# Kernel tuning notes

Hardware: AMD Instinct MI355X
Metric: run time of the kernel (lower is better)

The kernel has to match this reference:

```python
import jax, jax.numpy as jnp
import numpy as np

NUM_ENTS = 20000
NUM_RELS = 500
DIM = 256
BATCH = 32
GAMMA = 12.0
EPSILON = 2.0
EMB_RANGE = (GAMMA + EPSILON) / DIM  # embedding_range
PI = 3.1415926235897933


def setup_inputs() -> dict:
    key = jax.random.key(0)
    k1, k2, k3, k4 = jax.random.split(key, 4)
    # xavier_normal for 2-D params: std = sqrt(2/(fan_in+fan_out))
    std_e = float(np.sqrt(2.0 / (NUM_ENTS + 2 * DIM)))
    std_r = float(np.sqrt(2.0 / (NUM_RELS + 3 * DIM)))
    emb_e = jax.random.normal(k1, (NUM_ENTS, 2 * DIM), dtype=jnp.float32) * std_e
    emb_rel = jax.random.normal(k2, (NUM_RELS, 3 * DIM), dtype=jnp.float32) * std_r
    e1 = jax.random.randint(k3, (BATCH,), 0, NUM_ENTS, dtype=jnp.int32)
    rel = jax.random.randint(k4, (BATCH,), 0, NUM_RELS, dtype=jnp.int32)
    e2_multi = jax.random.uniform(jax.random.fold_in(key, 7), (BATCH, NUM_ENTS), dtype=jnp.float32)
    phase_weight = jnp.full((1, 1), 0.5 * EMB_RANGE, dtype=jnp.float32)
    modulus_weight = jnp.full((1, 1), 1.0, dtype=jnp.float32)
    return {
        "g": 0,
        "e1": e1,
        "rel": rel,
        "e2_multi": e2_multi,
        "emb_e": emb_e,
        "emb_rel": emb_rel,
        "phase_weight": phase_weight,
        "modulus_weight": modulus_weight,
    }


def reference(g, e1, rel, e2_multi, emb_e, emb_rel, phase_weight, modulus_weight):
    head = emb_e[e1]            # (B, 2D)
    r = emb_rel[rel]            # (B, 3D)
    tail = emb_e                # (N, 2D)

    phase_head, mod_head = jnp.split(head, 2, axis=-1)            # (B, D) each
    phase_rel, mod_rel, bias_rel = jnp.split(r, 3, axis=-1)       # (B, D) each
    phase_tail, mod_tail = jnp.split(tail, 2, axis=-1)            # (N, D) each

    scale = EMB_RANGE / PI
    phase_head = phase_head / scale
    phase_rel = phase_rel / scale
    phase_tail = phase_tail / scale

    # (B, N, D) broadcast
    phase_score = (phase_head + phase_rel)[:, None, :] - phase_tail[None, :, :]

    mod_rel = jnp.abs(mod_rel)
    bias_rel = jnp.minimum(bias_rel, 1.0)
    bias_rel = jnp.where(bias_rel < -mod_rel, -mod_rel, bias_rel)

    r_score = (mod_head * (mod_rel + bias_rel))[:, None, :] \
        - mod_tail[None, :, :] * (1.0 - bias_rel)[:, None, :]      # (B, N, D)

    phase_term = jnp.sum(jnp.abs(jnp.sin(phase_score / 2.0)), axis=-1) * phase_weight  # (B, N)
    r_term = jnp.linalg.norm(r_score, axis=-1) * modulus_weight                          # (B, N)

    return jax.nn.sigmoid(GAMMA - (phase_term + r_term))
```

## Files before the change

### kernel.cpp

```cpp
#include <hip/hip_runtime.h>
#include <math.h>


#define D_   256
#define N_   20000
#define NT   16
#define NBLK (N_ / NT)

#define K2S 4.571428571428571f

#define WS_A1 0
#define WS_A2 16384
#define WS_SC 32768
#define WS_S0 65536

typedef short short8 __attribute__((ext_vector_type(8)));
typedef float f32x4  __attribute__((ext_vector_type(4)));
typedef _Float16 half2_t __attribute__((ext_vector_type(2)));

union PKH { unsigned u; half2_t h; };

__device__ __forceinline__ float sinrev_(float x) { return __builtin_amdgcn_sinf(x); }
__device__ __forceinline__ float cosrev_(float x) { return __builtin_amdgcn_cosf(x); }

__device__ __forceinline__ unsigned short bf16r(float x) {
    union { float f; unsigned u; } v; v.f = x;
    return (unsigned short)((v.u + 0x7FFFu + ((v.u >> 16) & 1u)) >> 16);
}

__device__ __forceinline__ short8 pack8(float4 a, float4 b, bool sq) {
    float v[8] = {a.x, a.y, a.z, a.w, b.x, b.y, b.z, b.w};
    short8 r;
#pragma unroll
    for (int i = 0; i < 8; ++i) { float x = sq ? v[i] * v[i] : v[i]; r[i] = (short)bf16r(x); }
    return r;
}

__global__ __launch_bounds__(256)
void hake_prep(const int* __restrict__ e1, const int* __restrict__ rel,
               const float* __restrict__ emb_e, const float* __restrict__ emb_rel,
               char* __restrict__ ws)
{
    __shared__ float sp[4];
    const int b = blockIdx.x, d = threadIdx.x;
    const int he = e1[b], hr = rel[b];
    const float ph = emb_e[(size_t)he * 512 + d];
    const float mh = emb_e[(size_t)he * 512 + 256 + d];
    const float pr = emb_rel[(size_t)hr * 768 + d];
    const float mr = emb_rel[(size_t)hr * 768 + 256 + d];
    const float bi = emb_rel[(size_t)hr * 768 + 512 + d];

    const float a = (ph + pr) * K2S;
    PKH x;
    x.h.x = (_Float16)(-cosrev_(a));
    x.h.y = (_Float16)(sinrev_(a));
    ((unsigned*)(ws + WS_SC))[b * 256 + d] = x.u;

    const float mra = fabsf(mr);
    float bic = fminf(bi, 1.0f);
    bic = (bic < -mra) ? -mra : bic;
    const float cc  = 1.0f - bic;
    const float mhp = mh * (mra + bic);
    ((short*)(ws + WS_A1))[b * 256 + d] = (short)bf16r(cc * cc);
    ((short*)(ws + WS_A2))[b * 256 + d] = (short)bf16r(-2.0f * mhp * cc);

    float s0 = mhp * mhp;
#pragma unroll
    for (int o = 1; o < 64; o <<= 1) s0 += __shfl_xor(s0, o, 64);
    if ((threadIdx.x & 63) == 0) sp[threadIdx.x >> 6] = s0;
    __syncthreads();
    if (threadIdx.x == 0)
        ((float*)(ws + WS_S0))[b] = sp[0] + sp[1] + sp[2] + sp[3];
}

__global__ __launch_bounds__(512, 8)
void hake_main(const float* __restrict__ emb_e,
               const char* __restrict__ ws,
               const float* __restrict__ pw_p, const float* __restrict__ mw_p,
               float* __restrict__ out)
{
    __shared__ unsigned Pb[NT * 256];
    __shared__ float U[4352];

    const int t   = threadIdx.x;
    const int l   = t & 63;
    const int w   = t >> 6;
    const int b   = t & 31;
    const int g   = t >> 5;
    const int dlo = g * 16;
    const int fr  = l & 15;
    const int hi  = l >> 4;
    const int n0  = blockIdx.x * NT;

    const short*    A1w = (const short*)(ws + WS_A1);
    const short*    A2w = (const short*)(ws + WS_A2);
    const unsigned* SCw = (const unsigned*)(ws + WS_SC);
    const float*    S0w = (const float*)(ws + WS_S0);

    const int term  = w >> 2;
    const int dbase = (w & 3) * 64;
    const float* mtp = emb_e + (size_t)(n0 + fr) * (2 * D_) + D_;
    float4 bva0 = *(const float4*)(mtp + dbase + hi * 8);
    float4 bvb0 = *(const float4*)(mtp + dbase + hi * 8 + 4);
    float4 bva1 = *(const float4*)(mtp + dbase + 32 + hi * 8);
    float4 bvb1 = *(const float4*)(mtp + dbase + 32 + hi * 8 + 4);

    const float* prow0 = emb_e + (size_t)(n0 + w * 2) * (2 * D_);
    const float* prow1 = emb_e + (size_t)(n0 + w * 2 + 1) * (2 * D_);
    float2 lp00 = *(const float2*)(prow0 + 2 * l);
    float2 lp01 = *(const float2*)(prow0 + 128 + 2 * l);
    float2 lp10 = *(const float2*)(prow1 + 2 * l);
    float2 lp11 = *(const float2*)(prow1 + 128 + 2 * l);

    const short* At = term ? A2w : A1w;
    short8 a00 = *(const short8*)(At + fr * 256 + dbase + hi * 8);
    short8 a01 = *(const short8*)(At + fr * 256 + dbase + 32 + hi * 8);
    short8 a10 = *(const short8*)(At + (16 + fr) * 256 + dbase + hi * 8);
    short8 a11 = *(const short8*)(At + (16 + fr) * 256 + dbase + 32 + hi * 8);

    {
        PKH w0, w1;
        float v0, v1;
        v0 = lp00.x * K2S; v1 = lp00.y * K2S;
        w0.h.x = (_Float16)sinrev_(v0); w0.h.y = (_Float16)cosrev_(v0);
        w1.h.x = (_Float16)sinrev_(v1); w1.h.y = (_Float16)cosrev_(v1);
        *(uint2*)(&Pb[(w * 2) * 256 + 2 * l]) = make_uint2(w0.u, w1.u);
        v0 = lp01.x * K2S; v1 = lp01.y * K2S;
        w0.h.x = (_Float16)sinrev_(v0); w0.h.y = (_Float16)cosrev_(v0);
        w1.h.x = (_Float16)sinrev_(v1); w1.h.y = (_Float16)cosrev_(v1);
        *(uint2*)(&Pb[(w * 2) * 256 + 128 + 2 * l]) = make_uint2(w0.u, w1.u);
        v0 = lp10.x * K2S; v1 = lp10.y * K2S;
        w0.h.x = (_Float16)sinrev_(v0); w0.h.y = (_Float16)cosrev_(v0);
        w1.h.x = (_Float16)sinrev_(v1); w1.h.y = (_Float16)cosrev_(v1);
        *(uint2*)(&Pb[(w * 2 + 1) * 256 + 2 * l]) = make_uint2(w0.u, w1.u);
        v0 = lp11.x * K2S; v1 = lp11.y * K2S;
        w0.h.x = (_Float16)sinrev_(v0); w0.h.y = (_Float16)cosrev_(v0);
        w1.h.x = (_Float16)sinrev_(v1); w1.h.y = (_Float16)cosrev_(v1);
        *(uint2*)(&Pb[(w * 2 + 1) * 256 + 128 + 2 * l]) = make_uint2(w0.u, w1.u);
    }

    {
        short8 bf0 = pack8(bva0, bvb0, term == 0);
        short8 bf1 = pack8(bva1, bvb1, term == 0);
        f32x4 acc0 = {0.f, 0.f, 0.f, 0.f};
        f32x4 acc1 = {0.f, 0.f, 0.f, 0.f};
        acc0 = __builtin_amdgcn_mfma_f32_16x16x32_bf16(a00, bf0, acc0, 0, 0, 0);
        acc0 = __builtin_amdgcn_mfma_f32_16x16x32_bf16(a01, bf1, acc0, 0, 0, 0);
        acc1 = __builtin_amdgcn_mfma_f32_16x16x32_bf16(a10, bf0, acc1, 0, 0, 0);
        acc1 = __builtin_amdgcn_mfma_f32_16x16x32_bf16(a11, bf1, acc1, 0, 0, 0);
#pragma unroll
        for (int r = 0; r < 4; ++r) {
            U[(w * 32 + hi * 4 + r) * 17 + fr]      = acc0[r];
            U[(w * 32 + 16 + hi * 4 + r) * 17 + fr] = acc1[r];
        }
    }
    __syncthreads();

    const int fn = t >> 5, fb = t & 31;
    float rr = 0.0f;
#pragma unroll
    for (int ww = 0; ww < 8; ++ww) rr += U[(ww * 32 + fb) * 17 + fn];

    half2_t Xr[16];
    {
        uint4 s0 = *(const uint4*)(SCw + b * 256 + dlo);
        uint4 s1 = *(const uint4*)(SCw + b * 256 + dlo + 4);
        uint4 s2 = *(const uint4*)(SCw + b * 256 + dlo + 8);
        uint4 s3 = *(const uint4*)(SCw + b * 256 + dlo + 12);
        Xr[0]  = __builtin_bit_cast(half2_t, s0.x);
        Xr[1]  = __builtin_bit_cast(half2_t, s0.y);
        Xr[2]  = __builtin_bit_cast(half2_t, s0.z);
        Xr[3]  = __builtin_bit_cast(half2_t, s0.w);
        Xr[4]  = __builtin_bit_cast(half2_t, s1.x);
        Xr[5]  = __builtin_bit_cast(half2_t, s1.y);
        Xr[6]  = __builtin_bit_cast(half2_t, s1.z);
        Xr[7]  = __builtin_bit_cast(half2_t, s1.w);
        Xr[8]  = __builtin_bit_cast(half2_t, s2.x);
        Xr[9]  = __builtin_bit_cast(half2_t, s2.y);
        Xr[10] = __builtin_bit_cast(half2_t, s2.z);
        Xr[11] = __builtin_bit_cast(half2_t, s2.w);
        Xr[12] = __builtin_bit_cast(half2_t, s3.x);
        Xr[13] = __builtin_bit_cast(half2_t, s3.y);
        Xr[14] = __builtin_bit_cast(half2_t, s3.z);
        Xr[15] = __builtin_bit_cast(half2_t, s3.w);
    }

    float sph[NT];
#pragma unroll
    for (int j = 0; j < NT; ++j) sph[j] = 0.0f;

#pragma unroll
    for (int q = 0; q < 4; ++q) {
        const half2_t x0 = Xr[q * 4 + 0];
        const half2_t x1 = Xr[q * 4 + 1];
        const half2_t x2 = Xr[q * 4 + 2];
        const half2_t x3 = Xr[q * 4 + 3];
#pragma unroll
        for (int j = 0; j < NT; ++j) {
            uint4 tv = *(const uint4*)(&Pb[j * 256 + dlo + q * 4]);
            sph[j] += fabsf(__builtin_amdgcn_fdot2(x0, __builtin_bit_cast(half2_t, tv.x), 0.0f, false));
            sph[j] += fabsf(__builtin_amdgcn_fdot2(x1, __builtin_bit_cast(half2_t, tv.y), 0.0f, false));
            sph[j] += fabsf(__builtin_amdgcn_fdot2(x2, __builtin_bit_cast(half2_t, tv.z), 0.0f, false));
            sph[j] += fabsf(__builtin_amdgcn_fdot2(x3, __builtin_bit_cast(half2_t, tv.w), 0.0f, false));
        }
    }

#pragma unroll
    for (int j = 0; j < NT; ++j) sph[j] += __shfl_xor(sph[j], 32, 64);
    __syncthreads();
    if (l < 32) {
#pragma unroll
        for (int j = 0; j < NT; ++j) U[(w * 16 + j) * 32 + l] = sph[j];
    }
    __syncthreads();

    {
        float pa = 0.0f;
#pragma unroll
        for (int ww = 0; ww < 8; ++ww) pa += U[(ww * 16 + fn) * 32 + fb];
        float rfull = fmaxf(rr + S0w[fb], 0.0f);
        float z = fmaf(pa, pw_p[0], sqrtf(rfull) * mw_p[0]) - 12.0f;
        out[(size_t)fb * N_ + (n0 + fn)] = 1.0f / (1.0f + __expf(z));
    }
}

extern "C" void kernel_launch(void* const* d_in, const int* in_sizes, int n_in,
                              void* d_out, int out_size, void* d_ws, size_t ws_size,
                              hipStream_t stream)
{
    const int*   e1      = (const int*)d_in[1];
    const int*   rel     = (const int*)d_in[2];
    const float* emb_e   = (const float*)d_in[4];
    const float* emb_rel = (const float*)d_in[5];
    const float* pw      = (const float*)d_in[6];
    const float* mw      = (const float*)d_in[7];
    float* out = (float*)d_out;

    hipLaunchKernelGGL(hake_prep, dim3(32), dim3(256), 0, stream,
                       e1, rel, emb_e, emb_rel, (char*)d_ws);
    hipLaunchKernelGGL(hake_main, dim3(NBLK), dim3(512), 0, stream,
                       emb_e, (const char*)d_ws, pw, mw, out);
}
```

Baseline: 35.40 us.

## Move modulus MFMA GEMM into a separate kernel and transpose the phase workspace

The modulus term (bf16 MFMA over the tail modulus against A1/A2) moves out of hake_main into a new hake_rgemm kernel. That kernel does the full K=256 reduction per 16-row wave, adds S0, and writes a 32xN result matrix to workspace; hake_main then just prefetches one value per thread. The per-batch phase vectors are stored transposed so each thread loads its Xr registers with coalesced scalar loads. The aim is a lighter main kernel with fewer shared-memory reductions and one fewer barrier, paid for with an extra launch and a roughly 2.5 MB global write and read round trip. The phase reduction now uses float4 stores to a stride-17 shared array, which may be misaligned.

```diff
diff --git a/kernel.cpp b/kernel.cpp
--- a/kernel.cpp
+++ b/kernel.cpp
@@ -11,8 +11,9 @@
 
 #define WS_A1 0
 #define WS_A2 16384
-#define WS_SC 32768
+#define WS_XT 32768
 #define WS_S0 65536
+#define WS_R  65792
 
 typedef short short8 __attribute__((ext_vector_type(8)));
 typedef float f32x4  __attribute__((ext_vector_type(4)));
@@ -54,7 +55,7 @@
     PKH x;
     x.h.x = (_Float16)(-cosrev_(a));
     x.h.y = (_Float16)(sinrev_(a));
-    ((unsigned*)(ws + WS_SC))[b * 256 + d] = x.u;
+    ((unsigned*)(ws + WS_XT))[d * 32 + b] = x.u;
 
     const float mra = fabsf(mr);
     float bic = fminf(bi, 1.0f);
@@ -73,6 +74,50 @@
         ((float*)(ws + WS_S0))[b] = sp[0] + sp[1] + sp[2] + sp[3];
 }
 
+__global__ __launch_bounds__(256)
+void hake_rgemm(const float* __restrict__ emb_e, char* __restrict__ ws)
+{
+    const int t = threadIdx.x;
+    const int w = t >> 6, l = t & 63;
+    const int n0 = blockIdx.x * 64 + w * 16;
+    if (n0 >= N_) return;
+
+    const short* A1w = (const short*)(ws + WS_A1);
+    const short* A2w = (const short*)(ws + WS_A2);
+    const float* S0w = (const float*)(ws + WS_S0);
+    float*       Rw  = (float*)(ws + WS_R);
+
+    const int fr   = l & 15;
+    const int koff = (l >> 4) * 8;
+    const float* mtp = emb_e + (size_t)(n0 + fr) * (2 * D_) + D_;
+
+    f32x4 acc0 = {0.f, 0.f, 0.f, 0.f};
+    f32x4 acc1 = {0.f, 0.f, 0.f, 0.f};
+#pragma unroll
+    for (int ch = 0; ch < 8; ++ch) {
+        const int d = ch * 32 + koff;
+        float4 va = *(const float4*)(mtp + d);
+        float4 vb = *(const float4*)(mtp + d + 4);
+        short8 b2f = pack8(va, vb, false);
+        short8 b1f = pack8(va, vb, true);
+        short8 a1_0 = *(const short8*)(A1w + fr * 256 + d);
+        short8 a2_0 = *(const short8*)(A2w + fr * 256 + d);
+        short8 a1_1 = *(const short8*)(A1w + (16 + fr) * 256 + d);
+        short8 a2_1 = *(const short8*)(A2w + (16 + fr) * 256 + d);
+        acc0 = __builtin_amdgcn_mfma_f32_16x16x32_bf16(a1_0, b1f, acc0, 0, 0, 0);
+        acc0 = __builtin_amdgcn_mfma_f32_16x16x32_bf16(a2_0, b2f, acc0, 0, 0, 0);
+        acc1 = __builtin_amdgcn_mfma_f32_16x16x32_bf16(a1_1, b1f, acc1, 0, 0, 0);
+        acc1 = __builtin_amdgcn_mfma_f32_16x16x32_bf16(a2_1, b2f, acc1, 0, 0, 0);
+    }
+
+#pragma unroll
+    for (int r = 0; r < 4; ++r) {
+        const int row = (l >> 4) * 4 + r;
+        Rw[(size_t)row * N_ + n0 + fr]        = acc0[r] + S0w[row];
+        Rw[(size_t)(16 + row) * N_ + n0 + fr] = acc1[r] + S0w[16 + row];
+    }
+}
+
 __global__ __launch_bounds__(512, 8)
 void hake_main(const float* __restrict__ emb_e,
                const char* __restrict__ ws,
@@ -80,7 +125,7 @@
                float* __restrict__ out)
 {
     __shared__ unsigned Pb[NT * 256];
-    __shared__ float U[4352];
+    __shared__ float redf[8 * 32 * 17];
 
     const int t   = threadIdx.x;
     const int l   = t & 63;
@@ -88,22 +133,14 @@
     const int b   = t & 31;
     const int g   = t >> 5;
     const int dlo = g * 16;
-    const int fr  = l & 15;
-    const int hi  = l >> 4;
     const int n0  = blockIdx.x * NT;
 
-    const short*    A1w = (const short*)(ws + WS_A1);
-    const short*    A2w = (const short*)(ws + WS_A2);
-    const unsigned* SCw = (const unsigned*)(ws + WS_SC);
-    const float*    S0w = (const float*)(ws + WS_S0);
-
-    const int term  = w >> 2;
-    const int dbase = (w & 3) * 64;
-    const float* mtp = emb_e + (size_t)(n0 + fr) * (2 * D_) + D_;
-    float4 bva0 = *(const float4*)(mtp + dbase + hi * 8);
-    float4 bvb0 = *(const float4*)(mtp + dbase + hi * 8 + 4);
-    float4 bva1 = *(const float4*)(mtp + dbase + 32 + hi * 8);
-    float4 bvb1 = *(const float4*)(mtp + dbase + 32 + hi * 8 + 4);
+    const unsigned* XTw = (const unsigned*)(ws + WS_XT);
+    const float*    Rw  = (const float*)(ws + WS_R);
+
+    const int fn = t & 15, fb = t >> 4;
+
+    float rprefetch = Rw[(size_t)fb * N_ + n0 + fn];
 
     const float* prow0 = emb_e + (size_t)(n0 + w * 2) * (2 * D_);
     const float* prow1 = emb_e + (size_t)(n0 + w * 2 + 1) * (2 * D_);
@@ -112,11 +149,10 @@
     float2 lp10 = *(const float2*)(prow1 + 2 * l);
     float2 lp11 = *(const float2*)(prow1 + 128 + 2 * l);
 
-    const short* At = term ? A2w : A1w;
-    short8 a00 = *(const short8*)(At + fr * 256 + dbase + hi * 8);
-    short8 a01 = *(const short8*)(At + fr * 256 + dbase + 32 + hi * 8);
-    short8 a10 = *(const short8*)(At + (16 + fr) * 256 + dbase + hi * 8);
-    short8 a11 = *(const short8*)(At + (16 + fr) * 256 + dbase + 32 + hi * 8);
+    half2_t Xr[16];
+#pragma unroll
+    for (int i = 0; i < 16; ++i)
+        Xr[i] = __builtin_bit_cast(half2_t, XTw[(dlo + i) * 32 + b]);
 
     {
         PKH w0, w1;
@@ -138,52 +174,7 @@
         w1.h.x = (_Float16)sinrev_(v1); w1.h.y = (_Float16)cosrev_(v1);
         *(uint2*)(&Pb[(w * 2 + 1) * 256 + 128 + 2 * l]) = make_uint2(w0.u, w1.u);
     }
-
-    {
-        short8 bf0 = pack8(bva0, bvb0, term == 0);
-        short8 bf1 = pack8(bva1, bvb1, term == 0);
-        f32x4 acc0 = {0.f, 0.f, 0.f, 0.f};
-        f32x4 acc1 = {0.f, 0.f, 0.f, 0.f};
-        acc0 = __builtin_amdgcn_mfma_f32_16x16x32_bf16(a00, bf0, acc0, 0, 0, 0);
-        acc0 = __builtin_amdgcn_mfma_f32_16x16x32_bf16(a01, bf1, acc0, 0, 0, 0);
-        acc1 = __builtin_amdgcn_mfma_f32_16x16x32_bf16(a10, bf0, acc1, 0, 0, 0);
-        acc1 = __builtin_amdgcn_mfma_f32_16x16x32_bf16(a11, bf1, acc1, 0, 0, 0);
-#pragma unroll
-        for (int r = 0; r < 4; ++r) {
-            U[(w * 32 + hi * 4 + r) * 17 + fr]      = acc0[r];
-            U[(w * 32 + 16 + hi * 4 + r) * 17 + fr] = acc1[r];
-        }
-    }
     __syncthreads();
-
-    const int fn = t >> 5, fb = t & 31;
-    float rr = 0.0f;
-#pragma unroll
-    for (int ww = 0; ww < 8; ++ww) rr += U[(ww * 32 + fb) * 17 + fn];
-
-    half2_t Xr[16];
-    {
-        uint4 s0 = *(const uint4*)(SCw + b * 256 + dlo);
-        uint4 s1 = *(const uint4*)(SCw + b * 256 + dlo + 4);
-        uint4 s2 = *(const uint4*)(SCw + b * 256 + dlo + 8);
-        uint4 s3 = *(const uint4*)(SCw + b * 256 + dlo + 12);
-        Xr[0]  = __builtin_bit_cast(half2_t, s0.x);
-        Xr[1]  = __builtin_bit_cast(half2_t, s0.y);
-        Xr[2]  = __builtin_bit_cast(half2_t, s0.z);
-        Xr[3]  = __builtin_bit_cast(half2_t, s0.w);
-        Xr[4]  = __builtin_bit_cast(half2_t, s1.x);
-        Xr[5]  = __builtin_bit_cast(half2_t, s1.y);
-        Xr[6]  = __builtin_bit_cast(half2_t, s1.z);
-        Xr[7]  = __builtin_bit_cast(half2_t, s1.w);
-        Xr[8]  = __builtin_bit_cast(half2_t, s2.x);
-        Xr[9]  = __builtin_bit_cast(half2_t, s2.y);
-        Xr[10] = __builtin_bit_cast(half2_t, s2.z);
-        Xr[11] = __builtin_bit_cast(half2_t, s2.w);
-        Xr[12] = __builtin_bit_cast(half2_t, s3.x);
-        Xr[13] = __builtin_bit_cast(half2_t, s3.y);
-        Xr[14] = __builtin_bit_cast(half2_t, s3.z);
-        Xr[15] = __builtin_bit_cast(half2_t, s3.w);
-    }
 
     float sph[NT];
 #pragma unroll
@@ -207,18 +198,20 @@
 
 #pragma unroll
     for (int j = 0; j < NT; ++j) sph[j] += __shfl_xor(sph[j], 32, 64);
-    __syncthreads();
     if (l < 32) {
-#pragma unroll
-        for (int j = 0; j < NT; ++j) U[(w * 16 + j) * 32 + l] = sph[j];
+        float4* dst = (float4*)&redf[(w * 32 + l) * 17];
+#pragma unroll
+        for (int qq = 0; qq < 4; ++qq)
+            dst[qq] = make_float4(sph[qq * 4 + 0], sph[qq * 4 + 1],
+                                  sph[qq * 4 + 2], sph[qq * 4 + 3]);
     }
     __syncthreads();
 
     {
         float pa = 0.0f;
 #pragma unroll
-        for (int ww = 0; ww < 8; ++ww) pa += U[(ww * 16 + fn) * 32 + fb];
-        float rfull = fmaxf(rr + S0w[fb], 0.0f);
+        for (int ww = 0; ww < 8; ++ww) pa += redf[(ww * 32 + fb) * 17 + fn];
+        float rfull = fmaxf(rprefetch, 0.0f);
         float z = fmaf(pa, pw_p[0], sqrtf(rfull) * mw_p[0]) - 12.0f;
         out[(size_t)fb * N_ + (n0 + fn)] = 1.0f / (1.0f + __expf(z));
     }
@@ -238,6 +231,8 @@
 
     hipLaunchKernelGGL(hake_prep, dim3(32), dim3(256), 0, stream,
                        e1, rel, emb_e, emb_rel, (char*)d_ws);
+    hipLaunchKernelGGL(hake_rgemm, dim3(313), dim3(256), 0, stream,
+                       emb_e, (char*)d_ws);
     hipLaunchKernelGGL(hake_main, dim3(NBLK), dim3(512), 0, stream,
                        emb_e, (const char*)d_ws, pw, mw, out);
 }
```

Result: slower. 116.9 us (+230.2%).

## Register-block phase term as 4x4 batch-by-entity tiles with transposed layouts

Applied to the files above, without the earlier changes.

The phase-term loop now gives each thread a 4x4 tile of (batch, entity) outputs per 16-dim slice. Head sin/cos values are stored transposed in the workspace (d-major) and tail values transposed in shared memory with padding, so each load feeds 16 dot products instead of one. The goal is fewer LDS reads per fdot2 and lower register pressure than keeping 16 head values and 16 accumulators per thread. In exchange it changes the output-to-thread mapping for the final reduction, drops the occupancy hint, and uses a non-unrolled d-loop that reads the head values from global memory on every iteration.

```diff
diff --git a/kernel.cpp b/kernel.cpp
--- a/kernel.cpp
+++ b/kernel.cpp
@@ -11,7 +11,7 @@
 
 #define WS_A1 0
 #define WS_A2 16384
-#define WS_SC 32768
+#define WS_XT 32768
 #define WS_S0 65536
 
 typedef short short8 __attribute__((ext_vector_type(8)));
@@ -22,6 +22,7 @@
 
 __device__ __forceinline__ float sinrev_(float x) { return __builtin_amdgcn_sinf(x); }
 __device__ __forceinline__ float cosrev_(float x) { return __builtin_amdgcn_cosf(x); }
+__device__ __forceinline__ half2_t h2_(unsigned u) { return __builtin_bit_cast(half2_t, u); }
 
 __device__ __forceinline__ unsigned short bf16r(float x) {
     union { float f; unsigned u; } v; v.f = x;
@@ -34,6 +35,11 @@
 #pragma unroll
     for (int i = 0; i < 8; ++i) { float x = sq ? v[i] * v[i] : v[i]; r[i] = (short)bf16r(x); }
     return r;
+}
+
+__device__ __forceinline__ unsigned packsc_(float v) {
+    PKH p; p.h.x = (_Float16)sinrev_(v); p.h.y = (_Float16)cosrev_(v);
+    return p.u;
 }
 
 __global__ __launch_bounds__(256)
@@ -54,7 +60,7 @@
     PKH x;
     x.h.x = (_Float16)(-cosrev_(a));
     x.h.y = (_Float16)(sinrev_(a));
-    ((unsigned*)(ws + WS_SC))[b * 256 + d] = x.u;
+    ((unsigned*)(ws + WS_XT))[d * 32 + b] = x.u;
 
     const float mra = fabsf(mr);
     float bic = fminf(bi, 1.0f);
@@ -73,75 +79,67 @@
         ((float*)(ws + WS_S0))[b] = sp[0] + sp[1] + sp[2] + sp[3];
 }
 
-__global__ __launch_bounds__(512, 8)
+__global__ __launch_bounds__(512)
 void hake_main(const float* __restrict__ emb_e,
                const char* __restrict__ ws,
                const float* __restrict__ pw_p, const float* __restrict__ mw_p,
                float* __restrict__ out)
 {
-    __shared__ unsigned Pb[NT * 256];
-    __shared__ float U[4352];
+    __shared__ unsigned Pt[256 * 17];
+    __shared__ float U[8 * 32 * 17];
 
     const int t   = threadIdx.x;
     const int l   = t & 63;
     const int w   = t >> 6;
-    const int b   = t & 31;
     const int g   = t >> 5;
+    const int lg  = t & 31;
+    const int bq  = lg >> 2;
+    const int jq  = lg & 3;
     const int dlo = g * 16;
-    const int fr  = l & 15;
-    const int hi  = l >> 4;
     const int n0  = blockIdx.x * NT;
 
     const short*    A1w = (const short*)(ws + WS_A1);
     const short*    A2w = (const short*)(ws + WS_A2);
-    const unsigned* SCw = (const unsigned*)(ws + WS_SC);
+    const unsigned* XTw = (const unsigned*)(ws + WS_XT);
     const float*    S0w = (const float*)(ws + WS_S0);
 
     const int term  = w >> 2;
     const int dbase = (w & 3) * 64;
+    const int fr    = l & 15;
+    const int hi    = l >> 4;
     const float* mtp = emb_e + (size_t)(n0 + fr) * (2 * D_) + D_;
     float4 bva0 = *(const float4*)(mtp + dbase + hi * 8);
     float4 bvb0 = *(const float4*)(mtp + dbase + hi * 8 + 4);
     float4 bva1 = *(const float4*)(mtp + dbase + 32 + hi * 8);
     float4 bvb1 = *(const float4*)(mtp + dbase + 32 + hi * 8 + 4);
 
-    const float* prow0 = emb_e + (size_t)(n0 + w * 2) * (2 * D_);
-    const float* prow1 = emb_e + (size_t)(n0 + w * 2 + 1) * (2 * D_);
-    float2 lp00 = *(const float2*)(prow0 + 2 * l);
-    float2 lp01 = *(const float2*)(prow0 + 128 + 2 * l);
-    float2 lp10 = *(const float2*)(prow1 + 2 * l);
-    float2 lp11 = *(const float2*)(prow1 + 128 + 2 * l);
-
-    const short* At = term ? A2w : A1w;
-    short8 a00 = *(const short8*)(At + fr * 256 + dbase + hi * 8);
-    short8 a01 = *(const short8*)(At + fr * 256 + dbase + 32 + hi * 8);
-    short8 a10 = *(const short8*)(At + (16 + fr) * 256 + dbase + hi * 8);
-    short8 a11 = *(const short8*)(At + (16 + fr) * 256 + dbase + 32 + hi * 8);
-
     {
-        PKH w0, w1;
-        float v0, v1;
-        v0 = lp00.x * K2S; v1 = lp00.y * K2S;
-        w0.h.x = (_Float16)sinrev_(v0); w0.h.y = (_Float16)cosrev_(v0);
-        w1.h.x = (_Float16)sinrev_(v1); w1.h.y = (_Float16)cosrev_(v1);
-        *(uint2*)(&Pb[(w * 2) * 256 + 2 * l]) = make_uint2(w0.u, w1.u);
-        v0 = lp01.x * K2S; v1 = lp01.y * K2S;
-        w0.h.x = (_Float16)sinrev_(v0); w0.h.y = (_Float16)cosrev_(v0);
-        w1.h.x = (_Float16)sinrev_(v1); w1.h.y = (_Float16)cosrev_(v1);
-        *(uint2*)(&Pb[(w * 2) * 256 + 128 + 2 * l]) = make_uint2(w0.u, w1.u);
-        v0 = lp10.x * K2S; v1 = lp10.y * K2S;
-        w0.h.x = (_Float16)sinrev_(v0); w0.h.y = (_Float16)cosrev_(v0);
-        w1.h.x = (_Float16)sinrev_(v1); w1.h.y = (_Float16)cosrev_(v1);
-        *(uint2*)(&Pb[(w * 2 + 1) * 256 + 2 * l]) = make_uint2(w0.u, w1.u);
-        v0 = lp11.x * K2S; v1 = lp11.y * K2S;
-        w0.h.x = (_Float16)sinrev_(v0); w0.h.y = (_Float16)cosrev_(v0);
-        w1.h.x = (_Float16)sinrev_(v1); w1.h.y = (_Float16)cosrev_(v1);
-        *(uint2*)(&Pb[(w * 2 + 1) * 256 + 128 + 2 * l]) = make_uint2(w0.u, w1.u);
+        const int j0 = w * 2;
+        const float* prow0 = emb_e + (size_t)(n0 + j0) * (2 * D_);
+        const float* prow1 = emb_e + (size_t)(n0 + j0 + 1) * (2 * D_);
+        float2 lp00 = *(const float2*)(prow0 + 2 * l);
+        float2 lp01 = *(const float2*)(prow0 + 128 + 2 * l);
+        float2 lp10 = *(const float2*)(prow1 + 2 * l);
+        float2 lp11 = *(const float2*)(prow1 + 128 + 2 * l);
+
+        Pt[(2 * l) * 17 + j0]           = packsc_(lp00.x * K2S);
+        Pt[(2 * l + 1) * 17 + j0]       = packsc_(lp00.y * K2S);
+        Pt[(128 + 2 * l) * 17 + j0]     = packsc_(lp01.x * K2S);
+        Pt[(128 + 2 * l + 1) * 17 + j0] = packsc_(lp01.y * K2S);
+        Pt[(2 * l) * 17 + j0 + 1]           = packsc_(lp10.x * K2S);
+        Pt[(2 * l + 1) * 17 + j0 + 1]       = packsc_(lp10.y * K2S);
+        Pt[(128 + 2 * l) * 17 + j0 + 1]     = packsc_(lp11.x * K2S);
+        Pt[(128 + 2 * l + 1) * 17 + j0 + 1] = packsc_(lp11.y * K2S);
     }
 
     {
+        const short* At = term ? A2w : A1w;
         short8 bf0 = pack8(bva0, bvb0, term == 0);
         short8 bf1 = pack8(bva1, bvb1, term == 0);
+        short8 a00 = *(const short8*)(At + fr * 256 + dbase + hi * 8);
+        short8 a01 = *(const short8*)(At + fr * 256 + dbase + 32 + hi * 8);
+        short8 a10 = *(const short8*)(At + (16 + fr) * 256 + dbase + hi * 8);
+        short8 a11 = *(const short8*)(At + (16 + fr) * 256 + dbase + 32 + hi * 8);
         f32x4 acc0 = {0.f, 0.f, 0.f, 0.f};
         f32x4 acc1 = {0.f, 0.f, 0.f, 0.f};
         acc0 = __builtin_amdgcn_mfma_f32_16x16x32_bf16(a00, bf0, acc0, 0, 0, 0);
@@ -156,68 +154,54 @@
     }
     __syncthreads();
 
-    const int fn = t >> 5, fb = t & 31;
+    const int fn = t & 15, fb = t >> 4;
     float rr = 0.0f;
 #pragma unroll
     for (int ww = 0; ww < 8; ++ww) rr += U[(ww * 32 + fb) * 17 + fn];
 
-    half2_t Xr[16];
+    float acc[4][4];
+#pragma unroll
+    for (int bi = 0; bi < 4; ++bi)
+#pragma unroll
+        for (int ji = 0; ji < 4; ++ji) acc[bi][ji] = 0.0f;
+
+#pragma unroll 1
+    for (int dd = 0; dd < 16; ++dd) {
+        const int d = dlo + dd;
+        uint4 xv = *(const uint4*)(XTw + d * 32 + bq * 4);
+        uint4 pv = *(const uint4*)(&Pt[d * 17 + jq * 4]);
+        const unsigned xs[4] = {xv.x, xv.y, xv.z, xv.w};
+        const unsigned ps[4] = {pv.x, pv.y, pv.z, pv.w};
+#pragma unroll
+        for (int bi = 0; bi < 4; ++bi) {
+#pragma unroll
+            for (int ji = 0; ji < 4; ++ji) {
+                acc[bi][ji] += fabsf(__builtin_amdgcn_fdot2(h2_(xs[bi]), h2_(ps[ji]), 0.0f, false));
+            }
+        }
+    }
+
+#pragma unroll
+    for (int bi = 0; bi < 4; ++bi)
+#pragma unroll
+        for (int ji = 0; ji < 4; ++ji)
+            acc[bi][ji] += __shfl_xor(acc[bi][ji], 32, 64);
+    __syncthreads();
+    if (l < 32) {
+#pragma unroll
+        for (int bi = 0; bi < 4; ++bi)
+#pragma unroll
+            for (int ji = 0; ji < 4; ++ji)
+                U[(w * 32 + lg) * 17 + bi * 4 + ji] = acc[bi][ji];
+    }
+    __syncthreads();
+
     {
-        uint4 s0 = *(const uint4*)(SCw + b * 256 + dlo);
-        uint4 s1 = *(const uint4*)(SCw + b * 256 + dlo + 4);
-        uint4 s2 = *(const uint4*)(SCw + b * 256 + dlo + 8);
-        uint4 s3 = *(const uint4*)(SCw + b * 256 + dlo + 12);
-        Xr[0]  = __builtin_bit_cast(half2_t, s0.x);
-        Xr[1]  = __builtin_bit_cast(half2_t, s0.y);
-        Xr[2]  = __builtin_bit_cast(half2_t, s0.z);
-        Xr[3]  = __builtin_bit_cast(half2_t, s0.w);
-        Xr[4]  = __builtin_bit_cast(half2_t, s1.x);
-        Xr[5]  = __builtin_bit_cast(half2_t, s1.y);
-        Xr[6]  = __builtin_bit_cast(half2_t, s1.z);
-        Xr[7]  = __builtin_bit_cast(half2_t, s1.w);
-        Xr[8]  = __builtin_bit_cast(half2_t, s2.x);
-        Xr[9]  = __builtin_bit_cast(half2_t, s2.y);
-        Xr[10] = __builtin_bit_cast(half2_t, s2.z);
-        Xr[11] = __builtin_bit_cast(half2_t, s2.w);
-        Xr[12] = __builtin_bit_cast(half2_t, s3.x);
-        Xr[13] = __builtin_bit_cast(half2_t, s3.y);
-        Xr[14] = __builtin_bit_cast(half2_t, s3.z);
-        Xr[15] = __builtin_bit_cast(half2_t, s3.w);
-    }
-
-    float sph[NT];
-#pragma unroll
-    for (int j = 0; j < NT; ++j) sph[j] = 0.0f;
-
-#pragma unroll
-    for (int q = 0; q < 4; ++q) {
-        const half2_t x0 = Xr[q * 4 + 0];
-        const half2_t x1 = Xr[q * 4 + 1];
-        const half2_t x2 = Xr[q * 4 + 2];
-        const half2_t x3 = Xr[q * 4 + 3];
-#pragma unroll
-        for (int j = 0; j < NT; ++j) {
-            uint4 tv = *(const uint4*)(&Pb[j * 256 + dlo + q * 4]);
-            sph[j] += fabsf(__builtin_amdgcn_fdot2(x0, __builtin_bit_cast(half2_t, tv.x), 0.0f, false));
-            sph[j] += fabsf(__builtin_amdgcn_fdot2(x1, __builtin_bit_cast(half2_t, tv.y), 0.0f, false));
-            sph[j] += fabsf(__builtin_amdgcn_fdot2(x2, __builtin_bit_cast(half2_t, tv.z), 0.0f, false));
-            sph[j] += fabsf(__builtin_amdgcn_fdot2(x3, __builtin_bit_cast(half2_t, tv.w), 0.0f, false));
-        }
-    }
-
-#pragma unroll
-    for (int j = 0; j < NT; ++j) sph[j] += __shfl_xor(sph[j], 32, 64);
-    __syncthreads();
-    if (l < 32) {
-#pragma unroll
-        for (int j = 0; j < NT; ++j) U[(w * 16 + j) * 32 + l] = sph[j];
-    }
-    __syncthreads();
-
-    {
+        const int lgk = (fb >> 2) * 4 + (fn >> 2);
+        const int k   = (fb & 3) * 4 + (fn & 3);
         float pa = 0.0f;
 #pragma unroll
-        for (int ww = 0; ww < 8; ++ww) pa += U[(ww * 16 + fn) * 32 + fb];
+        for (int ww = 0; ww < 8; ++ww) pa += U[(ww * 32 + lgk) * 17 + k];
         float rfull = fmaxf(rr + S0w[fb], 0.0f);
         float z = fmaf(pa, pw_p[0], sqrtf(rfull) * mw_p[0]) - 12.0f;
         out[(size_t)fb * N_ + (n0 + fn)] = 1.0f / (1.0f + __expf(z));
```

New measurement: 38.72 us. 9.4% more time.
